# Kernel optimization log

Measured on AMD Instinct MI355X. Metric: run time of the kernel, lower is better.

The kernel has to match this reference:

```python
import jax, jax.numpy as jnp
import numpy as np

NUM_HEADS = 32
NUM_KV_HEADS = 8
HEAD_DIM = 128
ROPE_THETA = 10000.0
MAX_SEQ_LEN = 2048


def build_rope_cache(seq_len, head_dim, theta=10000.0):
    freq_indices = jnp.arange(0, head_dim, 2, dtype=jnp.float32)
    inv_freq = 1.0 / theta ** (freq_indices / head_dim)
    positions = jnp.arange(seq_len, dtype=jnp.float32)
    angles = jnp.outer(positions, inv_freq)  # (S, D/2)
    cos = jnp.cos(angles)
    sin = jnp.sin(angles)
    return jnp.concatenate([cos, cos], axis=-1), jnp.concatenate([sin, sin], axis=-1)


def apply_rotary_embedding(x, cos, sin):
    # x: (B, S, H, D); cos/sin: (S, D)
    d = x.shape[-1]
    x1, x2 = x[..., : d // 2], x[..., d // 2 :]
    x_rot = jnp.concatenate([-x2, x1], axis=-1)
    return x * cos[None, :, None, :] + x_rot * sin[None, :, None, :]


def setup_inputs() -> dict:
    key = jax.random.key(0)
    k_x, k_q, k_k, k_v, k_o = jax.random.split(key, 5)
    B, S, HID = 2, 2048, NUM_HEADS * HEAD_DIM
    KV = NUM_KV_HEADS * HEAD_DIM
    x = jax.random.normal(k_x, (B, S, HID), dtype=jnp.float32)
    # causal mask, shape (B, 1, S, S)
    causal = jnp.tril(jnp.ones((S, S), dtype=bool))
    mask = jnp.broadcast_to(causal[None, None], (B, 1, S, S))
    sc_in = 1.0 / np.sqrt(HID)
    Wq = jax.random.normal(k_q, (HID, HID), dtype=jnp.float32) * sc_in
    Wk = jax.random.normal(k_k, (HID, KV), dtype=jnp.float32) * sc_in
    Wv = jax.random.normal(k_v, (HID, KV), dtype=jnp.float32) * sc_in
    Wo = jax.random.normal(k_o, (HID, HID), dtype=jnp.float32) * sc_in
    return {"x": x, "mask": mask, "Wq": Wq, "Wk": Wk, "Wv": Wv, "Wo": Wo}


def reference(x, mask, Wq, Wk, Wv, Wo):
    B, S, _ = x.shape
    q = (x @ Wq).reshape(B, S, NUM_HEADS, HEAD_DIM)
    k = (x @ Wk).reshape(B, S, NUM_KV_HEADS, HEAD_DIM)
    v = (x @ Wv).reshape(B, S, NUM_KV_HEADS, HEAD_DIM)
    cos, sin = build_rope_cache(MAX_SEQ_LEN, HEAD_DIM, ROPE_THETA)
    cos, sin = cos[:S], sin[:S]
    q = apply_rotary_embedding(q, cos, sin)
    k = apply_rotary_embedding(k, cos, sin)
    group = NUM_HEADS // NUM_KV_HEADS
    if group > 1:
        k = jnp.repeat(k, group, axis=2)
        v = jnp.repeat(v, group, axis=2)
    scale = HEAD_DIM ** -0.5
    # (B, H, S, S)
    scores = jnp.einsum("bqhd,bkhd->bhqk", q, k) * scale
    scores = jnp.where(mask, scores, jnp.finfo(jnp.float32).min)
    attn = jax.nn.softmax(scores, axis=-1)
    out = jnp.einsum("bhqk,bkhd->bqhd", attn, v).reshape(B, S, NUM_HEADS * HEAD_DIM)
    return out @ Wo
```

## Files before the change

### kernel.cpp

```cpp
#include <hip/hip_runtime.h>

#define S_LEN   2048
#define HID_DIM 4096
#define NHEADS  32
#define NKVH    8
#define HD      128
#define KV_DIM  1024
#define KV2     2048
#define BS_ROWS 4096

typedef __attribute__((ext_vector_type(4))) float f32x4;
typedef __attribute__((ext_vector_type(8))) short bf16x8;

__device__ __forceinline__ unsigned short f2b(float f) {
  union { float f; unsigned int u; } cv; cv.f = f;
  unsigned int r = (cv.u + 0x7FFFu + ((cv.u >> 16) & 1u)) >> 16;
  return (unsigned short)r;
}
__device__ __forceinline__ float b2f(unsigned short u) {
  union { unsigned int u; float f; } cv; cv.u = ((unsigned int)u) << 16; return cv.f;
}
__device__ __forceinline__ void gload_lds16(const void* g, void* l) {
  __builtin_amdgcn_global_load_lds(
      (const __attribute__((address_space(1))) unsigned int*)g,
      (__attribute__((address_space(3))) unsigned int*)l, 16, 0, 0);
}
__device__ __forceinline__ void store_out(float* p, float v) { *p = v; }
__device__ __forceinline__ void store_out(unsigned short* p, float v) { *p = f2b(v); }

__global__ void cvt_f32_bf16(const float* __restrict__ in, unsigned short* __restrict__ out, int n4) {
  int i = blockIdx.x * blockDim.x + threadIdx.x;
  if (i >= n4) return;
  f32x4 v = reinterpret_cast<const f32x4*>(in)[i];
  ushort4 o;
  o.x = f2b(v[0]); o.y = f2b(v[1]); o.z = f2b(v[2]); o.w = f2b(v[3]);
  reinterpret_cast<ushort4*>(out)[i] = o;
}

__global__ void transpose_cvt(const float* __restrict__ W, unsigned short* __restrict__ Wt,
                              int K, int N) {
  __shared__ float t[32][33];
  int n0 = blockIdx.x * 32, k0 = blockIdx.y * 32;
  int tx = threadIdx.x, ty = threadIdx.y;
#pragma unroll
  for (int i = 0; i < 4; ++i)
    t[ty + 8 * i][tx] = W[(size_t)(k0 + ty + 8 * i) * N + n0 + tx];
  __syncthreads();
#pragma unroll
  for (int i = 0; i < 4; ++i)
    Wt[(size_t)(n0 + ty + 8 * i) * K + k0 + tx] = f2b(t[tx][ty + 8 * i]);
}

__global__ void transpose_v_k(const unsigned short* __restrict__ KVb, unsigned short* __restrict__ Vt) {
  __shared__ unsigned short t[32][33];
  int c0 = blockIdx.x * 32;
  int r0 = blockIdx.y * 32;
  int tx = threadIdx.x, ty = threadIdx.y;
#pragma unroll
  for (int i = 0; i < 4; ++i)
    t[ty + 8 * i][tx] = KVb[(size_t)(r0 + ty + 8 * i) * KV2 + KV_DIM + c0 + tx];
  __syncthreads();
  int ob = (r0 >> 11) * 1024;
  int oc = r0 & 2047;
#pragma unroll
  for (int i = 0; i < 4; ++i)
    Vt[(size_t)(ob + c0 + ty + 8 * i) * S_LEN + oc + tx] = t[tx][ty + 8 * i];
}

__global__ void rope_table_k(float* __restrict__ cosT, float* __restrict__ sinT) {
  int idx = blockIdx.x * blockDim.x + threadIdx.x;
  if (idx >= S_LEN * 64) return;
  int s = idx >> 6, i = idx & 63;
  float inv = 1.0f / powf(10000.0f, (float)(2 * i) * (1.0f / 128.0f));
  float ang = (float)s * inv;
  cosT[idx] = cosf(ang);
  sinT[idx] = sinf(ang);
}

__global__ void rope_apply_k(unsigned short* __restrict__ X, const float* __restrict__ cosT,
                             const float* __restrict__ sinT, int nheads, int rowstride,
                             float scale, int total) {
  int idx = blockIdx.x * blockDim.x + threadIdx.x;
  if (idx >= total) return;
  int i4 = idx & 15;
  int t = idx >> 4;
  int h = t % nheads;
  int row = t / nheads;
  int s = row & (S_LEN - 1);
  f32x4 c4 = *reinterpret_cast<const f32x4*>(&cosT[(s << 6) + i4 * 4]);
  f32x4 s4 = *reinterpret_cast<const f32x4*>(&sinT[(s << 6) + i4 * 4]);
  size_t base = (size_t)row * rowstride + (size_t)h * HD + i4 * 4;
  ushort4 xa = *reinterpret_cast<const ushort4*>(&X[base]);
  ushort4 xb = *reinterpret_cast<const ushort4*>(&X[base + 64]);
  unsigned short* pa = (unsigned short*)&xa;
  unsigned short* pb = (unsigned short*)&xb;
  ushort4 oa, ob;
  unsigned short* qa = (unsigned short*)&oa;
  unsigned short* qb = (unsigned short*)&ob;
#pragma unroll
  for (int j = 0; j < 4; ++j) {
    float x1 = b2f(pa[j]), x2 = b2f(pb[j]);
    qa[j] = f2b((x1 * c4[j] - x2 * s4[j]) * scale);
    qb[j] = f2b((x2 * c4[j] + x1 * s4[j]) * scale);
  }
  *reinterpret_cast<ushort4*>(&X[base])      = oa;
  *reinterpret_cast<ushort4*>(&X[base + 64]) = ob;
}

template <typename OutT>
__global__ __launch_bounds__(256) void gemm_bt(const unsigned short* __restrict__ A,
                                               const unsigned short* __restrict__ Bt,
                                               OutT* __restrict__ C, int M, int N, int K) {
  __shared__ unsigned short As[128 * 32];
  __shared__ unsigned short Bs[128 * 32];
  const int tid = threadIdx.x;
  const int lane = tid & 63;
  const int wave = tid >> 6;
  int nwg = gridDim.x, wg = blockIdx.x;
  int swz = (nwg % 8 == 0) ? ((wg & 7) * (nwg >> 3) + (wg >> 3)) : wg;
  const int nbn = N >> 7;
  const int bm = swz / nbn, bn = swz % nbn;
  const int m0 = bm << 7, n0 = bn << 7;
  const int wr = wave >> 1, wc = wave & 1;
  const int lr = lane & 15, kb = lane >> 4;

  f32x4 acc[4][4];
#pragma unroll
  for (int i = 0; i < 4; ++i)
#pragma unroll
    for (int j = 0; j < 4; ++j) acc[i][j] = (f32x4){0.f, 0.f, 0.f, 0.f};

  const unsigned short* Ab = A + (size_t)m0 * K;
  const unsigned short* Bb = Bt + (size_t)n0 * K;

  for (int k0 = 0; k0 < K; k0 += 32) {
    __syncthreads();
#pragma unroll
    for (int i = 0; i < 2; ++i) {
      int idx = i * 256 + tid;
      int row = idx >> 2;
      int off = (idx & 3) << 3;
      gload_lds16(Ab + (size_t)row * K + k0 + off, As + row * 32 + off);
      gload_lds16(Bb + (size_t)row * K + k0 + off, Bs + row * 32 + off);
    }
    __syncthreads();

    bf16x8 af[4], bfr[4];
#pragma unroll
    for (int mi = 0; mi < 4; ++mi)
      af[mi] = *reinterpret_cast<const bf16x8*>(As + (wr * 64 + mi * 16 + lr) * 32 + kb * 8);
#pragma unroll
    for (int ni = 0; ni < 4; ++ni)
      bfr[ni] = *reinterpret_cast<const bf16x8*>(Bs + (wc * 64 + ni * 16 + lr) * 32 + kb * 8);
#pragma unroll
    for (int mi = 0; mi < 4; ++mi)
#pragma unroll
      for (int ni = 0; ni < 4; ++ni)
        acc[mi][ni] = __builtin_amdgcn_mfma_f32_16x16x32_bf16(af[mi], bfr[ni], acc[mi][ni], 0, 0, 0);
  }

#pragma unroll
  for (int mi = 0; mi < 4; ++mi)
#pragma unroll
    for (int ni = 0; ni < 4; ++ni)
#pragma unroll
      for (int r = 0; r < 4; ++r) {
        int row = m0 + wr * 64 + mi * 16 + kb * 4 + r;
        int col = n0 + wc * 64 + ni * 16 + lr;
        store_out(&C[(size_t)row * N + col], acc[mi][ni][r]);
      }
}

#define STAGE_HALF(dstBase, Sp, k0, h)                                           \
  {                                                                              \
    _Pragma("unroll")                                                            \
    for (int i_ = 0; i_ < 2; ++i_) {                                             \
      int c_ = i_ * 512 + tid;                                                   \
      int rl_ = c_ >> 3, ch_ = c_ & 7;                                           \
      int row_ = (h) * 128 + rl_;                                                \
      gload_lds16((Sp) + (size_t)row_ * K + (k0) + ((ch_ ^ (row_ & 7)) << 3),    \
                  (char*)(dstBase) + row_ * 128 + ch_ * 16);                     \
    }                                                                            \
  }
#define LDF(buf, R, sw) \
  (*reinterpret_cast<const bf16x8*>((const char*)(buf) + (R) * 128 + (sw)))
#define PHASE_SYNC()                                        \
  __builtin_amdgcn_s_barrier();                             \
  asm volatile("s_waitcnt lgkmcnt(0)" ::: "memory");        \
  __builtin_amdgcn_sched_barrier(0);

template <typename OutT>
__global__ __launch_bounds__(512, 1) void gemm256(const unsigned short* __restrict__ A,
                                                  const unsigned short* __restrict__ Bt,
                                                  OutT* __restrict__ C, int M, int N, int K) {
  __shared__ unsigned short Asl[2][256 * 64];
  __shared__ unsigned short Bsl[2][256 * 64];
  const int tid = threadIdx.x;
  const int lane = tid & 63;
  const int wave = tid >> 6;
  const int wr = wave >> 2;
  const int wc = wave & 3;
  const int lr = lane & 15, kb = lane >> 4;

  int nwg = gridDim.x, wg = blockIdx.x;
  int swz = (nwg % 8 == 0) ? ((wg & 7) * (nwg >> 3) + (wg >> 3)) : wg;
  const int nbn = N >> 8;
  const int bm = swz / nbn, bn = swz % nbn;
  const int m0 = bm << 8, n0 = bn << 8;

  const unsigned short* Ab = A + (size_t)m0 * K;
  const unsigned short* Bb = Bt + (size_t)n0 * K;

  f32x4 acc[8][4];
#pragma unroll
  for (int i = 0; i < 8; ++i)
#pragma unroll
    for (int j = 0; j < 4; ++j) acc[i][j] = (f32x4){0.f, 0.f, 0.f, 0.f};

  const int sw0 = ((kb) ^ (lr & 7)) << 4;
  const int sw1 = ((4 + kb) ^ (lr & 7)) << 4;

  STAGE_HALF(Asl[0], Ab, 0, 0); STAGE_HALF(Asl[0], Ab, 0, 1);
  STAGE_HALF(Bsl[0], Bb, 0, 0); STAGE_HALF(Bsl[0], Bb, 0, 1);
  __syncthreads();

  const int nt = K >> 6;
  bf16x8 af[4], bfr[4];

#pragma unroll 1
  for (int t = 0; t < nt; ++t) {
    const unsigned short* Acur = Asl[t & 1];
    const unsigned short* Bcur = Bsl[t & 1];
    unsigned short* Anxt = Asl[(t + 1) & 1];
    unsigned short* Bnxt = Bsl[(t + 1) & 1];
    const int k0n = (t + 1) << 6;
    const bool pf = (t + 1 < nt);

#pragma unroll
    for (int ni = 0; ni < 4; ++ni) bfr[ni] = LDF(Bcur, wc * 64 + ni * 16 + lr, sw0);
#pragma unroll
    for (int mi = 0; mi < 4; ++mi) af[mi] = LDF(Acur, wr * 128 + mi * 16 + lr, sw0);
    if (pf) { STAGE_HALF(Anxt, Ab, k0n, 0); STAGE_HALF(Anxt, Ab, k0n, 1); }
    PHASE_SYNC();
    __builtin_amdgcn_s_setprio(1);
#pragma unroll
    for (int mi = 0; mi < 4; ++mi)
#pragma unroll
      for (int ni = 0; ni < 4; ++ni)
        acc[mi][ni] = __builtin_amdgcn_mfma_f32_16x16x32_bf16(af[mi], bfr[ni], acc[mi][ni], 0, 0, 0);
    __builtin_amdgcn_s_setprio(0);
    __builtin_amdgcn_s_barrier();

#pragma unroll
    for (int mi = 0; mi < 4; ++mi) af[mi] = LDF(Acur, wr * 128 + (mi + 4) * 16 + lr, sw0);
    if (pf) { STAGE_HALF(Bnxt, Bb, k0n, 0); STAGE_HALF(Bnxt, Bb, k0n, 1); }
    PHASE_SYNC();
    __builtin_amdgcn_s_setprio(1);
#pragma unroll
    for (int mi = 0; mi < 4; ++mi)
#pragma unroll
      for (int ni = 0; ni < 4; ++ni)
        acc[mi + 4][ni] = __builtin_amdgcn_mfma_f32_16x16x32_bf16(af[mi], bfr[ni], acc[mi + 4][ni], 0, 0, 0);
    __builtin_amdgcn_s_setprio(0);
    __builtin_amdgcn_s_barrier();

#pragma unroll
    for (int ni = 0; ni < 4; ++ni) bfr[ni] = LDF(Bcur, wc * 64 + ni * 16 + lr, sw1);
#pragma unroll
    for (int mi = 0; mi < 4; ++mi) af[mi] = LDF(Acur, wr * 128 + mi * 16 + lr, sw1);
    PHASE_SYNC();
    __builtin_amdgcn_s_setprio(1);
#pragma unroll
    for (int mi = 0; mi < 4; ++mi)
#pragma unroll
      for (int ni = 0; ni < 4; ++ni)
        acc[mi][ni] = __builtin_amdgcn_mfma_f32_16x16x32_bf16(af[mi], bfr[ni], acc[mi][ni], 0, 0, 0);
    __builtin_amdgcn_s_setprio(0);
    __builtin_amdgcn_s_barrier();

#pragma unroll
    for (int mi = 0; mi < 4; ++mi) af[mi] = LDF(Acur, wr * 128 + (mi + 4) * 16 + lr, sw1);
    PHASE_SYNC();
    __builtin_amdgcn_s_setprio(1);
#pragma unroll
    for (int mi = 0; mi < 4; ++mi)
#pragma unroll
      for (int ni = 0; ni < 4; ++ni)
        acc[mi + 4][ni] = __builtin_amdgcn_mfma_f32_16x16x32_bf16(af[mi], bfr[ni], acc[mi + 4][ni], 0, 0, 0);
    __builtin_amdgcn_s_setprio(0);
    __builtin_amdgcn_s_barrier();

    if (pf) asm volatile("s_waitcnt vmcnt(0)" ::: "memory");
    __builtin_amdgcn_s_barrier();
  }

#pragma unroll
  for (int mi = 0; mi < 8; ++mi)
#pragma unroll
    for (int ni = 0; ni < 4; ++ni)
#pragma unroll
      for (int r = 0; r < 4; ++r) {
        int row = m0 + wr * 128 + mi * 16 + kb * 4 + r;
        int col = n0 + wc * 64 + ni * 16 + lr;
        store_out(&C[(size_t)row * N + col], acc[mi][ni][r]);
      }
}

__global__ __launch_bounds__(256, 2) void attn_fwd(const unsigned short* __restrict__ Q,
                                                   const unsigned short* __restrict__ KV,
                                                   const unsigned short* __restrict__ Vt,
                                                   const float* __restrict__ cosT,
                                                   const float* __restrict__ sinT,
                                                   unsigned short* __restrict__ O) {
  __shared__ unsigned short Ks[64 * 128];
  __shared__ unsigned short Ps[4][2][16 * 72];
  const int tid = threadIdx.x, lane = tid & 63, wave = tid >> 6;
  const int lr = lane & 15, kb = lane >> 4;
  const int pr = blockIdx.x;
  const int bh = blockIdx.y;
  const int b = bh >> 5, h = bh & 31, kvh = h >> 2;
  const unsigned short* Qp = Q + (size_t)b * S_LEN * HID_DIM + (size_t)h * HD;
  const unsigned short* Kp = KV + (size_t)b * S_LEN * KV2 + (size_t)kvh * HD;
  const unsigned short* Vtp = Vt + (size_t)(b * 8 + kvh) * HD * S_LEN;
  unsigned short* Op = O + (size_t)b * S_LEN * HID_DIM + (size_t)h * HD;

#pragma unroll 1
  for (int pass = 0; pass < 2; ++pass) {
    const int qt = pass ? pr : 15 - pr;
    const int q0 = qt * 128;
    int qrowQ[2];
    qrowQ[0] = q0 + wave * 32 + lr;
    qrowQ[1] = q0 + wave * 32 + 16 + lr;

    bf16x8 qf[2][4];
#pragma unroll
    for (int qs = 0; qs < 2; ++qs) {
      const int qrow = qrowQ[qs];
      bf16x8 raw[4];
#pragma unroll
      for (int dc = 0; dc < 4; ++dc)
        raw[dc] = *reinterpret_cast<const bf16x8*>(Qp + (size_t)qrow * HID_DIM + dc * 32 + kb * 8);
      const float* ct = cosT + (qrow << 6) + kb * 8;
      const float* st = sinT + (qrow << 6) + kb * 8;
      f32x4 cv0 = *(const f32x4*)(ct),      cv1 = *(const f32x4*)(ct + 4);
      f32x4 cv2 = *(const f32x4*)(ct + 32), cv3 = *(const f32x4*)(ct + 36);
      f32x4 sv0 = *(const f32x4*)(st),      sv1 = *(const f32x4*)(st + 4);
      f32x4 sv2 = *(const f32x4*)(st + 32), sv3 = *(const f32x4*)(st + 36);
      const float sc = 0.08838834764831843f;
#pragma unroll
      for (int j = 0; j < 8; ++j) {
        const int jj = j & 3;
        float c0 = (j < 4) ? cv0[jj] : cv1[jj];
        float s0 = (j < 4) ? sv0[jj] : sv1[jj];
        float c1 = (j < 4) ? cv2[jj] : cv3[jj];
        float s1 = (j < 4) ? sv2[jj] : sv3[jj];
        float a1 = b2f((unsigned short)raw[0][j]), a2 = b2f((unsigned short)raw[2][j]);
        qf[qs][0][j] = (short)f2b((a1 * c0 - a2 * s0) * sc);
        qf[qs][2][j] = (short)f2b((a2 * c0 + a1 * s0) * sc);
        float b1 = b2f((unsigned short)raw[1][j]), b2x = b2f((unsigned short)raw[3][j]);
        qf[qs][1][j] = (short)f2b((b1 * c1 - b2x * s1) * sc);
        qf[qs][3][j] = (short)f2b((b2x * c1 + b1 * s1) * sc);
      }
    }

    f32x4 of[2][8];
#pragma unroll
    for (int qs = 0; qs < 2; ++qs)
#pragma unroll
      for (int i = 0; i < 8; ++i) of[qs][i] = (f32x4){0.f, 0.f, 0.f, 0.f};
    float mrow[2] = {-3.0e38f, -3.0e38f};
    float lrow[2] = {0.f, 0.f};

    const int nsteps = 2 * qt + 2;

#pragma unroll 1
    for (int t = 0; t < nsteps; ++t) {
      const int kv0 = t << 6;
      __syncthreads();
#pragma unroll
      for (int i = 0; i < 4; ++i) {
        int c = i * 256 + tid;
        int key = c >> 4;
        int ch = (c & 15) ^ (key & 7);
        gload_lds16(Kp + (size_t)(kv0 + key) * KV2 + ch * 8, Ks + c * 8);
      }
      bf16x8 vf[8];
#pragma unroll
      for (int dc2 = 0; dc2 < 8; ++dc2)
        vf[dc2] = *reinterpret_cast<const bf16x8*>(
            Vtp + (size_t)(dc2 * 16 + lr) * S_LEN + kv0 + kb * 8);
      __syncthreads();

      f32x4 sf[2][4];
#pragma unroll
      for (int qs = 0; qs < 2; ++qs)
#pragma unroll
        for (int ki = 0; ki < 4; ++ki) sf[qs][ki] = (f32x4){0.f, 0.f, 0.f, 0.f};
#pragma unroll
      for (int ki = 0; ki < 4; ++ki)
#pragma unroll
        for (int dc = 0; dc < 4; ++dc) {
          bf16x8 kf = *reinterpret_cast<const bf16x8*>(
              Ks + (ki * 16 + lr) * 128 + (((dc * 4 + kb) ^ (lr & 7)) << 3));
          sf[0][ki] = __builtin_amdgcn_mfma_f32_16x16x32_bf16(kf, qf[0][dc], sf[0][ki], 0, 0, 0);
          sf[1][ki] = __builtin_amdgcn_mfma_f32_16x16x32_bf16(kf, qf[1][dc], sf[1][ki], 0, 0, 0);
        }

#pragma unroll
      for (int qs = 0; qs < 2; ++qs) {
        if (kv0 + 63 > q0 + wave * 32 + qs * 16) {
          const int thr = qrowQ[qs] - kv0;
#pragma unroll
          for (int ki = 0; ki < 4; ++ki)
#pragma unroll
            for (int r = 0; r < 4; ++r)
              if (ki * 16 + kb * 4 + r > thr) sf[qs][ki][r] = -3.0e38f;
        }
      }

#pragma unroll
      for (int qs = 0; qs < 2; ++qs) {
        float m8 = -3.0e38f;
#pragma unroll
        for (int ki = 0; ki < 4; ++ki)
#pragma unroll
          for (int r = 0; r < 4; ++r) m8 = fmaxf(m8, sf[qs][ki][r]);
        m8 = fmaxf(m8, __shfl_xor(m8, 16));
        m8 = fmaxf(m8, __shfl_xor(m8, 32));
        if (__any(m8 > mrow[qs] + 8.0f)) {
          float mn = fmaxf(mrow[qs], m8);
          float corr = __expf(mrow[qs] - mn);
          lrow[qs] *= corr;
#pragma unroll
          for (int r = 0; r < 4; ++r) {
            float cr = __shfl(corr, kb * 4 + r);
#pragma unroll
            for (int dc2 = 0; dc2 < 8; ++dc2) of[qs][dc2][r] *= cr;
          }
          mrow[qs] = mn;
        }
        float rs = 0.f;
        ushort4 pw[4];
#pragma unroll
        for (int ki = 0; ki < 4; ++ki) {
          unsigned short* pp = (unsigned short*)&pw[ki];
#pragma unroll
          for (int r = 0; r < 4; ++r) {
            float p = __expf(sf[qs][ki][r] - mrow[qs]);
            rs += p;
            pp[r] = f2b(p);
          }
        }
        rs += __shfl_xor(rs, 16);
        rs += __shfl_xor(rs, 32);
        lrow[qs] += rs;
#pragma unroll
        for (int ki = 0; ki < 4; ++ki)
          *reinterpret_cast<ushort4*>(&Ps[wave][qs][lr * 72 + ki * 16 + kb * 4]) = pw[ki];
      }
      asm volatile("s_waitcnt lgkmcnt(0)" ::: "memory");
      __builtin_amdgcn_sched_barrier(0);

      {
        bf16x8 pf0 = *reinterpret_cast<const bf16x8*>(&Ps[wave][0][lr * 72 + kb * 8]);
        bf16x8 pf1 = *reinterpret_cast<const bf16x8*>(&Ps[wave][1][lr * 72 + kb * 8]);
#pragma unroll
        for (int dc2 = 0; dc2 < 8; ++dc2) {
          of[0][dc2] = __builtin_amdgcn_mfma_f32_16x16x32_bf16(pf0, vf[dc2], of[0][dc2], 0, 0, 0);
          of[1][dc2] = __builtin_amdgcn_mfma_f32_16x16x32_bf16(pf1, vf[dc2], of[1][dc2], 0, 0, 0);
        }
      }
#pragma unroll
      for (int dc2 = 0; dc2 < 8; ++dc2)
        vf[dc2] = *reinterpret_cast<const bf16x8*>(
            Vtp + (size_t)(dc2 * 16 + lr) * S_LEN + kv0 + 32 + kb * 8);
      {
        bf16x8 pf0 = *reinterpret_cast<const bf16x8*>(&Ps[wave][0][lr * 72 + 32 + kb * 8]);
        bf16x8 pf1 = *reinterpret_cast<const bf16x8*>(&Ps[wave][1][lr * 72 + 32 + kb * 8]);
#pragma unroll
        for (int dc2 = 0; dc2 < 8; ++dc2) {
          of[0][dc2] = __builtin_amdgcn_mfma_f32_16x16x32_bf16(pf0, vf[dc2], of[0][dc2], 0, 0, 0);
          of[1][dc2] = __builtin_amdgcn_mfma_f32_16x16x32_bf16(pf1, vf[dc2], of[1][dc2], 0, 0, 0);
        }
      }
    }

#pragma unroll
    for (int qs = 0; qs < 2; ++qs) {
      float linv[4];
#pragma unroll
      for (int r = 0; r < 4; ++r) linv[r] = 1.0f / __shfl(lrow[qs], kb * 4 + r);
#pragma unroll
      for (int dc2 = 0; dc2 < 8; ++dc2)
#pragma unroll
        for (int r = 0; r < 4; ++r) {
          int qg = q0 + wave * 32 + qs * 16 + kb * 4 + r;
          Op[(size_t)qg * HID_DIM + dc2 * 16 + lr] = f2b(of[qs][dc2][r] * linv[r]);
        }
    }
  }
}

extern "C" void kernel_launch(void* const* d_in, const int* in_sizes, int n_in,
                              void* d_out, int out_size, void* d_ws, size_t ws_size,
                              hipStream_t stream) {
  const float* x  = (const float*)d_in[0];
  const float* Wq = (const float*)d_in[2];
  const float* Wk = (const float*)d_in[3];
  const float* Wv = (const float*)d_in[4];
  const float* Wo = (const float*)d_in[5];
  float* out = (float*)d_out;

  char* ws = (char*)d_ws;
  unsigned short* xb  = (unsigned short*)(ws + 0);
  unsigned short* wtb = (unsigned short*)(ws + 33554432);
  unsigned short* wkt = (unsigned short*)(ws + 67108864);
  unsigned short* wvt = (unsigned short*)(ws + 75497472);
  unsigned short* Qb  = (unsigned short*)(ws + 83886080);
  unsigned short* KVb = (unsigned short*)(ws + 117440512);
  float* cosT = (float*)(ws + 134217728);
  float* sinT = (float*)(ws + 134742016);
  unsigned short* AO  = xb;
  unsigned short* Vtb = wkt;

  cvt_f32_bf16<<<16384, 256, 0, stream>>>(x, xb, (BS_ROWS * HID_DIM) / 4);
  transpose_cvt<<<dim3(128, 128), dim3(32, 8), 0, stream>>>(Wq, wtb, HID_DIM, HID_DIM);
  transpose_cvt<<<dim3(32, 128), dim3(32, 8), 0, stream>>>(Wk, wkt, HID_DIM, KV_DIM);
  transpose_cvt<<<dim3(32, 128), dim3(32, 8), 0, stream>>>(Wv, wvt, HID_DIM, KV_DIM);
  rope_table_k<<<512, 256, 0, stream>>>(cosT, sinT);

  gemm256<unsigned short><<<256, 512, 0, stream>>>(xb, wtb, Qb, BS_ROWS, HID_DIM, HID_DIM);
  gemm_bt<unsigned short><<<512, 256, 0, stream>>>(xb, wkt, KVb, BS_ROWS, KV2, HID_DIM);

  transpose_v_k<<<dim3(32, 128), dim3(32, 8), 0, stream>>>(KVb, Vtb);
  transpose_cvt<<<dim3(128, 128), dim3(32, 8), 0, stream>>>(Wo, wtb, HID_DIM, HID_DIM);

  rope_apply_k<<<2048, 256, 0, stream>>>(KVb, cosT, sinT, NKVH, KV2, 1.0f,
                                         BS_ROWS * NKVH * 16);

  attn_fwd<<<dim3(8, 64), 256, 0, stream>>>(Qb, KVb, Vtb, cosT, sinT, AO);

  gemm256<float><<<256, 512, 0, stream>>>(AO, wtb, out, BS_ROWS, HID_DIM, HID_DIM);
}
```

Before: 583.0 us.

## Double-buffer K tiles in LDS and switch softmax to exp2 with packed bf16

The attention kernel now keeps two LDS buffers for K and loads the next 64-key tile while the current one is being used. This replaces two barriers per step with a single barrier at the end of each step. The softmax scale folds in log2(e), so the exponentials use the hardware exp2 instruction and the rescale threshold is adjusted to match. Probabilities are converted with a packed bf16 convert and stored directly to LDS. The cost is twice the K LDS footprint, which may reduce occupancy, and the code relies on the trailing barrier to make the prefetched K visible.

After: 559.0 us. -4.1%, faster.

```diff
diff --git a/kernel.cpp b/kernel.cpp
--- a/kernel.cpp
+++ b/kernel.cpp
@@ -24,6 +24,18 @@
   __builtin_amdgcn_global_load_lds(
       (const __attribute__((address_space(1))) unsigned int*)g,
       (__attribute__((address_space(3))) unsigned int*)l, 16, 0, 0);
+}
+__device__ __forceinline__ float exp2fast(float x) {
+#if __has_builtin(__builtin_amdgcn_exp2f)
+  return __builtin_amdgcn_exp2f(x);
+#else
+  return exp2f(x);
+#endif
+}
+__device__ __forceinline__ unsigned cvtpk(float a, float b) {
+  unsigned r;
+  asm("v_cvt_pk_bf16_f32 %0, %1, %2" : "=v"(r) : "v"(a), "v"(b));
+  return r;
 }
 __device__ __forceinline__ void store_out(float* p, float v) { *p = v; }
 __device__ __forceinline__ void store_out(unsigned short* p, float v) { *p = f2b(v); }
@@ -312,7 +324,7 @@
                                                    const float* __restrict__ cosT,
                                                    const float* __restrict__ sinT,
                                                    unsigned short* __restrict__ O) {
-  __shared__ unsigned short Ks[64 * 128];
+  __shared__ unsigned short Ks[2][64 * 128];
   __shared__ unsigned short Ps[4][2][16 * 72];
   const int tid = threadIdx.x, lane = tid & 63, wave = tid >> 6;
   const int lr = lane & 15, kb = lane >> 4;
@@ -346,7 +358,7 @@
       f32x4 cv2 = *(const f32x4*)(ct + 32), cv3 = *(const f32x4*)(ct + 36);
       f32x4 sv0 = *(const f32x4*)(st),      sv1 = *(const f32x4*)(st + 4);
       f32x4 sv2 = *(const f32x4*)(st + 32), sv3 = *(const f32x4*)(st + 36);
-      const float sc = 0.08838834764831843f;
+      const float sc = 0.08838834764831843f * 1.4426950408889634f;
 #pragma unroll
       for (int j = 0; j < 8; ++j) {
         const int jj = j & 3;
@@ -373,23 +385,36 @@
 
     const int nsteps = 2 * qt + 2;
 
+#pragma unroll
+    for (int i = 0; i < 4; ++i) {
+      int c = i * 256 + tid;
+      int key = c >> 4;
+      int ch = (c & 15) ^ (key & 7);
+      gload_lds16(Kp + (size_t)key * KV2 + ch * 8, &Ks[0][0] + c * 8);
+    }
+    __syncthreads();
+
 #pragma unroll 1
     for (int t = 0; t < nsteps; ++t) {
       const int kv0 = t << 6;
-      __syncthreads();
-#pragma unroll
-      for (int i = 0; i < 4; ++i) {
-        int c = i * 256 + tid;
-        int key = c >> 4;
-        int ch = (c & 15) ^ (key & 7);
-        gload_lds16(Kp + (size_t)(kv0 + key) * KV2 + ch * 8, Ks + c * 8);
-      }
+      const unsigned short* Kcur = &Ks[t & 1][0];
+
       bf16x8 vf[8];
 #pragma unroll
       for (int dc2 = 0; dc2 < 8; ++dc2)
         vf[dc2] = *reinterpret_cast<const bf16x8*>(
             Vtp + (size_t)(dc2 * 16 + lr) * S_LEN + kv0 + kb * 8);
-      __syncthreads();
+
+      if (t + 1 < nsteps) {
+        unsigned short* Knxt = &Ks[(t + 1) & 1][0];
+#pragma unroll
+        for (int i = 0; i < 4; ++i) {
+          int c = i * 256 + tid;
+          int key = c >> 4;
+          int ch = (c & 15) ^ (key & 7);
+          gload_lds16(Kp + (size_t)(kv0 + 64 + key) * KV2 + ch * 8, Knxt + c * 8);
+        }
+      }
 
       f32x4 sf[2][4];
 #pragma unroll
@@ -401,7 +426,7 @@
 #pragma unroll
         for (int dc = 0; dc < 4; ++dc) {
           bf16x8 kf = *reinterpret_cast<const bf16x8*>(
-              Ks + (ki * 16 + lr) * 128 + (((dc * 4 + kb) ^ (lr & 7)) << 3));
+              Kcur + (ki * 16 + lr) * 128 + (((dc * 4 + kb) ^ (lr & 7)) << 3));
           sf[0][ki] = __builtin_amdgcn_mfma_f32_16x16x32_bf16(kf, qf[0][dc], sf[0][ki], 0, 0, 0);
           sf[1][ki] = __builtin_amdgcn_mfma_f32_16x16x32_bf16(kf, qf[1][dc], sf[1][ki], 0, 0, 0);
         }
@@ -427,9 +452,9 @@
           for (int r = 0; r < 4; ++r) m8 = fmaxf(m8, sf[qs][ki][r]);
         m8 = fmaxf(m8, __shfl_xor(m8, 16));
         m8 = fmaxf(m8, __shfl_xor(m8, 32));
-        if (__any(m8 > mrow[qs] + 8.0f)) {
+        if (__any(m8 > mrow[qs] + 11.5f)) {
           float mn = fmaxf(mrow[qs], m8);
-          float corr = __expf(mrow[qs] - mn);
+          float corr = exp2fast(mrow[qs] - mn);
           lrow[qs] *= corr;
 #pragma unroll
           for (int r = 0; r < 4; ++r) {
@@ -440,23 +465,21 @@
           mrow[qs] = mn;
         }
         float rs = 0.f;
-        ushort4 pw[4];
 #pragma unroll
         for (int ki = 0; ki < 4; ++ki) {
-          unsigned short* pp = (unsigned short*)&pw[ki];
-#pragma unroll
-          for (int r = 0; r < 4; ++r) {
-            float p = __expf(sf[qs][ki][r] - mrow[qs]);
-            rs += p;
-            pp[r] = f2b(p);
-          }
+          float p0 = exp2fast(sf[qs][ki][0] - mrow[qs]);
+          float p1 = exp2fast(sf[qs][ki][1] - mrow[qs]);
+          float p2 = exp2fast(sf[qs][ki][2] - mrow[qs]);
+          float p3 = exp2fast(sf[qs][ki][3] - mrow[qs]);
+          rs += (p0 + p1) + (p2 + p3);
+          uint2 w;
+          w.x = cvtpk(p0, p1);
+          w.y = cvtpk(p2, p3);
+          *reinterpret_cast<uint2*>(&Ps[wave][qs][lr * 72 + ki * 16 + kb * 4]) = w;
         }
         rs += __shfl_xor(rs, 16);
         rs += __shfl_xor(rs, 32);
         lrow[qs] += rs;
-#pragma unroll
-        for (int ki = 0; ki < 4; ++ki)
-          *reinterpret_cast<ushort4*>(&Ps[wave][qs][lr * 72 + ki * 16 + kb * 4]) = pw[ki];
       }
       asm volatile("s_waitcnt lgkmcnt(0)" ::: "memory");
       __builtin_amdgcn_sched_barrier(0);
@@ -483,6 +506,8 @@
           of[1][dc2] = __builtin_amdgcn_mfma_f32_16x16x32_bf16(pf1, vf[dc2], of[1][dc2], 0, 0, 0);
         }
       }
+
+      __syncthreads();
     }
 
 #pragma unroll
```
